# Kernel optimization log

Measured on AMD Instinct MI355X. Metric: run time of the kernel, lower is better.

## Reference

```python
import jax, jax.numpy as jnp
import numpy as np

B, N, F, D, H, L, K = 128, 128, 13, 256, 8, 8, 10
FF = 2 * D  # FFN / hidden width
HEAD = D // H


def setup_inputs() -> dict:
    key = jax.random.key(0)
    ks = iter(jax.random.split(key, 64))
    def nrm(shape, scale=0.02):
        return jax.random.normal(next(ks), shape, dtype=jnp.float32) * scale
    return {
        "input_features": jax.random.normal(next(ks), (B, N, F), dtype=jnp.float32),
        "input_points": jax.random.normal(next(ks), (B, N, 2), dtype=jnp.float32),
        "input_mask": jnp.ones((B, N, 1), dtype=jnp.float32),
        "input_time": jax.random.uniform(next(ks), (B, 1), dtype=jnp.float32),
        # get_encoding: Dense(2D, gelu) -> Dense(D, gelu)
        "enc_w1": nrm((F, FF)), "enc_b1": jnp.zeros((FF,), jnp.float32),
        "enc_w2": nrm((FF, D)), "enc_b2": jnp.zeros((D,), jnp.float32),
        # FourierProjection MLP (no bias, swish)
        "four_w1": nrm((D, FF)), "four_w2": nrm((FF, D)),
        # FiLM time projection (no bias)
        "time_w": nrm((D, FF)),
        # local KNN MLPs: round 0 input 2*F, round 1 input 2*D
        "loc1_w1": nrm((2 * F, FF)), "loc1_b1": jnp.zeros((FF,), jnp.float32),
        "loc1_w2": nrm((FF, D)), "loc1_b2": jnp.zeros((D,), jnp.float32),
        "loc2_w1": nrm((2 * D, FF)), "loc2_b1": jnp.zeros((FF,), jnp.float32),
        "loc2_w2": nrm((FF, D)), "loc2_b2": jnp.zeros((D,), jnp.float32),
        # transformer encoder layers, stacked over L
        "qkv_w": nrm((L, D, 3 * D)), "qkv_b": jnp.zeros((L, 3 * D), jnp.float32),
        "out_w": nrm((L, D, D)), "out_b": jnp.zeros((L, D), jnp.float32),
        "ln1_g": jnp.ones((L, D), jnp.float32), "ln1_b": jnp.zeros((L, D), jnp.float32),
        "ff1_w": nrm((L, D, FF)), "ff1_b": jnp.zeros((L, FF), jnp.float32),
        "ff2_w": nrm((L, FF, D)), "ff2_b": jnp.zeros((L, D), jnp.float32),
        "gamma": jnp.full((L, D), 1e-5, dtype=jnp.float32),
        "ln2_g": jnp.ones((L, D), jnp.float32), "ln2_b": jnp.zeros((L, D), jnp.float32),
    }


def _ln(x, g, b, eps=1e-5):
    m = jnp.mean(x, axis=-1, keepdims=True)
    v = jnp.var(x, axis=-1, keepdims=True)
    return (x - m) * jax.lax.rsqrt(v + eps) * g + b


def _fourier(t, w1, w2):
    # t: (B,1) -> (B,D)
    half = D // 2
    emb = np.log(10000.0) / (half - 1)
    freq = jnp.exp(-emb * jnp.arange(half, dtype=jnp.float32))
    angle = t * freq[None, :] * 1000.0  # (B, half)
    e = jnp.concatenate([jnp.sin(angle), jnp.cos(angle)], axis=-1)
    e = jax.nn.silu(e @ w1)
    return jax.nn.silu(e @ w2)


def _get_neighbors(points, feats, w1, b1, w2, b2):
    # points: (B,N,P), feats: (B,N,C) -> (B,N,D)
    r = jnp.sum(points * points, axis=-1)  # (B,N)
    d = r[:, :, None] - 2.0 * jnp.einsum('bnp,bmp->bnm', points, points) + r[:, None, :]
    _, idx = jax.lax.top_k(-d, K + 1)
    idx = idx[:, :, 1:]  # drop self, (B,N,K)
    knn = jax.vmap(lambda f, i: f[i])(feats, idx)  # (B,N,K,C)
    center = jnp.broadcast_to(feats[:, :, None, :], knn.shape)
    local = jnp.concatenate([knn - center, center], axis=-1)  # (B,N,K,2C)
    local = jax.nn.gelu(local @ w1 + b1)
    local = jax.nn.gelu(local @ w2 + b2)
    return jnp.mean(local, axis=2)


def _mha(x, mask, wqkv, bqkv, wo, bo):
    Bx, Nx, _ = x.shape
    qkv = x @ wqkv + bqkv
    q, k, v = jnp.split(qkv, 3, axis=-1)
    def heads(t):
        return t.reshape(Bx, Nx, H, HEAD).transpose(0, 2, 1, 3)
    q, k, v = heads(q), heads(k), heads(v)
    scores = jnp.einsum('bhqd,bhkd->bhqk', q, k) * (1.0 / np.sqrt(HEAD))
    keep = mask[:, None, None, :, 0] > 0  # (B,1,1,N)
    scores = jnp.where(keep, scores, -1e9)
    a = jax.nn.softmax(scores, axis=-1)
    o = jnp.einsum('bhqk,bhkd->bhqd', a, v).transpose(0, 2, 1, 3).reshape(Bx, Nx, D)
    return o @ wo + bo


def _pet(input_features, input_points, input_mask, input_time,
         enc_w1, enc_b1, enc_w2, enc_b2, four_w1, four_w2, time_w,
         loc1_w1, loc1_b1, loc1_w2, loc1_b2, loc2_w1, loc2_b1, loc2_w2, loc2_b2,
         qkv_w, qkv_b, out_w, out_b, ln1_g, ln1_b, ff1_w, ff1_b, ff2_w, ff2_b,
         gamma, ln2_g, ln2_b):
    # feature encoding (RandomDrop is identity at eval / feature_drop=0)
    enc = jax.nn.gelu(input_features @ enc_w1 + enc_b1)
    enc = jax.nn.gelu(enc @ enc_w2 + enc_b2)  # (B,N,D)
    # FiLM time conditioning
    t = _fourier(input_time, four_w1, four_w2)  # (B,D)
    t = t[:, None, :] * input_mask  # (B,N,D)
    scale, shift = jnp.split(t @ time_w, 2, axis=-1)
    enc = enc * (1.0 + scale) + shift
    # local KNN aggregation
    coord_shift = 999.0 * (1.0 - input_mask)  # (B,N,1)
    points = input_points[:, :, :2]
    lf = _get_neighbors(coord_shift + points, input_features, loc1_w1, loc1_b1, loc1_w2, loc1_b2)
    lf = _get_neighbors(coord_shift + lf, lf, loc2_w1, loc2_b1, loc2_w2, loc2_b2)
    enc = enc + lf
    skip = enc
    x = enc
    for i in range(L):
        res = x
        a = _mha(x, input_mask, qkv_w[i], qkv_b[i], out_w[i], out_b[i])
        x = _ln(res + a, ln1_g[i], ln1_b[i])
        res = x
        h = jax.nn.gelu(x @ ff1_w[i] + ff1_b[i])
        h = h @ ff2_w[i] + ff2_b[i]
        h = h * gamma[i] * input_mask  # LayerScale with mask
        x = _ln(res + h, ln2_g[i], ln2_b[i])
    return x + skip


def reference(input_features, input_points, input_mask, input_time,
              enc_w1, enc_b1, enc_w2, enc_b2, four_w1, four_w2, time_w,
              loc1_w1, loc1_b1, loc1_w2, loc1_b2, loc2_w1, loc2_b1, loc2_w2, loc2_b2,
              qkv_w, qkv_b, out_w, out_b, ln1_g, ln1_b, ff1_w, ff1_b, ff2_w, ff2_b,
              gamma, ln2_g, ln2_b):
    return _pet(input_features, input_points, input_mask, input_time,
                enc_w1, enc_b1, enc_w2, enc_b2, four_w1, four_w2, time_w,
                loc1_w1, loc1_b1, loc1_w2, loc1_b2, loc2_w1, loc2_b1, loc2_w2, loc2_b2,
                qkv_w, qkv_b, out_w, out_b, ln1_g, ln1_b, ff1_w, ff1_b, ff2_w, ff2_b,
                gamma, ln2_g, ln2_b)
```

## Files before the change

kernel.cpp:

```cpp
#include <hip/hip_runtime.h>
#include <hip/hip_bf16.h>
#include <cmath>

#define DEV_INLINE __device__ __forceinline__

constexpr int Bn = 128;
constexpr int Nn = 128;
constexpr int Fn = 13;
constexpr int Dn = 256;
constexpr int Ln = 8;
constexpr int Kn = 10;
constexpr int FFn = 512;
constexpr int Tn = Bn * Nn;
constexpr int Rn = Tn * Kn;

typedef __attribute__((ext_vector_type(4))) float f32x4;
typedef __attribute__((ext_vector_type(8))) short bf16x8;
typedef unsigned short us;

__device__ float g_x[Tn * Dn];
__device__ float g_skip[Tn * Dn];
__device__ float g_big[Tn * Dn];
__device__ float g_dm[Tn * Nn];
__device__ float g_u[Bn * FFn];
// ... 292 lines not shown
    us* Qs = (us*)(smem + 34816);
    us* Ks = (us*)(smem + 45056);
    us* Vt = (us*)(smem + 55296);
    float* msk = (float*)(smem + 64000);
    us* As = (us*)smem;
    us* Bs = (us*)(smem + 8192);
    int bh = blockIdx.x;
    int b = bh >> 3, h = bh & 7;
    int tid = threadIdx.x;
    int wave = tid >> 6, lane = tid & 63;
    int lm = lane & 15, quad = lane >> 4;
    int wm = wave << 5;
    int colu = (((lane & 3) ^ ((lane >> 2) & 3)) << 3);
    int r0 = (wave << 5) + (lane >> 2);
    const us* pa0 = xb + (size_t)(b * 128 + r0) * 256 + colu;
    const us* pa1 = xb + (size_t)(b * 128 + r0 + 16) * 256 + colu;
    int seg0 = wave, seg1 = wave + 4;
    int n0_ = seg0 * 16 + (lane >> 2);
    int n1_ = seg1 * 16 + (lane >> 2);
    int g0 = (n0_ >> 5) * 256 + h * 32 + (n0_ & 31);
    int g1 = (n1_ >> 5) * 256 + h * 32 + (n1_ & 31);
    const us* pb0 = Bt + (size_t)g0 * 256 + colu;
    const us* pb1 = Bt + (size_t)g1 * 256 + colu;
    auto lAs = (__attribute__((address_space(3))) us*)As;
    auto lBs = (__attribute__((address_space(3))) us*)Bs;
    int fcol = ((quad ^ (lm & 3)) << 3);
    f32x4 gacc[2][6] = {};
    for (int k0 = 0; k0 < 256; k0 += 32) {
        __syncthreads();
        GLOAD16(pa0 + k0, lAs + (wave << 10));
        GLOAD16(pa1 + k0, lAs + (wave << 10) + 512);
        GLOAD16(pb0 + k0, lBs + (seg0 << 9));
        if (wave < 2) GLOAD16(pb1 + k0, lBs + (seg1 << 9));
        __syncthreads();
        bf16x8 afr[2], bfr[6];
#pragma unroll
        for (int mf = 0; mf < 2; mf++)
            afr[mf] = *(const bf16x8*)&As[(wm + mf * 16 + lm) * 32 + fcol];
#pragma unroll
        for (int nf = 0; nf < 6; nf++)
            bfr[nf] = *(const bf16x8*)&Bs[(nf * 16 + lm) * 32 + fcol];
#pragma unroll
        for (int mf = 0; mf < 2; mf++)
#pragma unroll
            for (int nf = 0; nf < 6; nf++)
                gacc[mf][nf] = __builtin_amdgcn_mfma_f32_16x16x32_bf16(afr[mf], bfr[nf], gacc[mf][nf], 0, 0, 0);
    }
    float bvq[6];
#pragma unroll
    for (int nf = 0; nf < 6; nf++) {
        int n = nf * 16 + lm;
        bvq[nf] = bias[(n >> 5) * 256 + h * 32 + (n & 31)];
    }
    __syncthreads();
#pragma unroll
    for (int mf = 0; mf < 2; mf++) {
#pragma unroll
        for (int r = 0; r < 4; r++) {
            int row = wm + mf * 16 + (quad << 2) + r;
#pragma unroll
            for (int nf = 0; nf < 6; nf++) {
                us hv = f2b(gacc[mf][nf][r] + bvq[nf]);
                int n = nf * 16 + lm;
                if (nf < 2) Qs[row * 40 + n] = hv;
                else if (nf < 4) Ks[row * 40 + (n - 32)] = hv;
                else Vt[(n - 64) * 136 + row] = hv;
            }
        }
    }
    if (tid < 128) msk[tid] = mask[b * 128 + tid];
    __syncthreads();
    f32x4 acc[2][8] = {};
    {
        bf16x8 aq[2];
#pragma unroll
        for (int mf = 0; mf < 2; mf++)
            aq[mf] = *(const bf16x8*)&Qs[(wm + mf * 16 + lm) * 40 + (quad << 3)];
#pragma unroll
        for (int nf = 0; nf < 8; nf++) {
            bf16x8 bk = *(const bf16x8*)&Ks[(nf * 16 + lm) * 40 + (quad << 3)];
            acc[0][nf] = __builtin_amdgcn_mfma_f32_16x16x32_bf16(aq[0], bk, acc[0][nf], 0, 0, 0);
            acc[1][nf] = __builtin_amdgcn_mfma_f32_16x16x32_bf16(aq[1], bk, acc[1][nf], 0, 0, 0);
        }
    }
    {
        const float sc = 0.17677669529663687f;
        float mkc[8];
#pragma unroll
        for (int nf = 0; nf < 8; nf++) mkc[nf] = msk[nf * 16 + lm];
#pragma unroll
        for (int mf = 0; mf < 2; mf++) {
#pragma unroll
            for (int nf = 0; nf < 8; nf++)
#pragma unroll
                for (int r = 0; r < 4; r++) {
                    float s = acc[mf][nf][r];
                    acc[mf][nf][r] = mkc[nf] > 0.f ? s * sc : -1.0e9f;
                }
#pragma unroll
            for (int r = 0; r < 4; r++) {
                float m = acc[mf][0][r];
#pragma unroll
                for (int nf = 1; nf < 8; nf++) m = fmaxf(m, acc[mf][nf][r]);
                m = fmaxf(m, __shfl_xor(m, 1, 64));
                m = fmaxf(m, __shfl_xor(m, 2, 64));
                m = fmaxf(m, __shfl_xor(m, 4, 64));
                m = fmaxf(m, __shfl_xor(m, 8, 64));
                float s = 0.f;
#pragma unroll
                for (int nf = 0; nf < 8; nf++) {
                    float p = __expf(acc[mf][nf][r] - m);
                    acc[mf][nf][r] = p;
                    s += p;
                }
                s += __shfl_xor(s, 1, 64);
                s += __shfl_xor(s, 2, 64);
                s += __shfl_xor(s, 4, 64);
                s += __shfl_xor(s, 8, 64);
                float linv = __builtin_amdgcn_rcpf(s);
                int prow = wm + mf * 16 + (quad << 2) + r;
#pragma unroll
                for (int nf = 0; nf < 8; nf++)
                    Ps[prow * 136 + nf * 16 + lm] = f2b(acc[mf][nf][r] * linv);
            }
        }
    }
    __syncthreads();
    f32x4 oacc[2][2] = {};
    for (int kt = 0; kt < 4; kt++) {
        bf16x8 ap[2], bv[2];
#pragma unroll
        for (int mf = 0; mf < 2; mf++)
            ap[mf] = *(const bf16x8*)&Ps[(wm + mf * 16 + lm) * 136 + kt * 32 + (quad << 3)];
#pragma unroll
        for (int nf = 0; nf < 2; nf++)
            bv[nf] = *(const bf16x8*)&Vt[(nf * 16 + lm) * 136 + kt * 32 + (quad << 3)];
#pragma unroll
        for (int mf = 0; mf < 2; mf++)
#pragma unroll
            for (int nf = 0; nf < 2; nf++)
                oacc[mf][nf] = __builtin_amdgcn_mfma_f32_16x16x32_bf16(ap[mf], bv[nf], oacc[mf][nf], 0, 0, 0);
    }
#pragma unroll
    for (int mf = 0; mf < 2; mf++)
#pragma unroll
        for (int r = 0; r < 4; r++) {
            int row = wm + mf * 16 + (quad << 2) + r;
#pragma unroll
            for (int nf = 0; nf < 2; nf++)
                attb[(size_t)(b * 128 + row) * 256 + h * 32 + nf * 16 + lm] = f2b(oacc[mf][nf][r]);
        }
}

__global__ __launch_bounds__(512) void k_mglnff(const us* __restrict__ A,
                                                const us* __restrict__ Bt,
                                                const float* __restrict__ bias,
                                                const us* __restrict__ res,
                                                const float* __restrict__ lng,
                                                const float* __restrict__ lnb,
                                                const us* __restrict__ W1t,
                                                const float* __restrict__ b1,
                                                us* __restrict__ xbout,
                                                us* __restrict__ ffout) {
    __shared__ __align__(16) char smem[57856];
    us* xln = (us*)smem;
    us* As = (us*)(smem + 32768);
    us* Bs = (us*)(smem + 36864);
    us* Bs2 = (us*)(smem + 32768);
    float2* part = (float2*)(smem + 53248);
    float2* stat = (float2*)(smem + 57344);
    int tid = threadIdx.x;
    int m0 = blockIdx.x << 6;
    int wave = tid >> 6, lane = tid & 63;
    int wn = wave << 5;
    int lm = lane & 15, quad = lane >> 4;
    int colu = (((lane & 3) ^ ((lane >> 2) & 3)) << 3);
    int ar = (wave << 4) + (lane >> 2);
    int br = (wave << 5) + (lane >> 2);
    const us* pa = A + (size_t)(m0 + ar) * 256 + colu;
    const us* pb0 = Bt + (size_t)br * 256 + colu;
    const us* pb1 = Bt + (size_t)(br + 16) * 256 + colu;
    auto lAs = (__attribute__((address_space(3))) us*)As;
    auto lBs = (__attribute__((address_space(3))) us*)Bs;
    auto lBs2 = (__attribute__((address_space(3))) us*)Bs2;
    int fcol = ((quad ^ (lm & 3)) << 3);
    f32x4 acc[4][2] = {};
    for (int k0 = 0; k0 < 256; k0 += 32) {
        __syncthreads();
        if (wave < 4) GLOAD16(pa + k0, lAs + (wave << 9));
        GLOAD16(pb0 + k0, lBs + (wave << 10));
        GLOAD16(pb1 + k0, lBs + (wave << 10) + 512);
        __syncthreads();
        bf16x8 afr[4], bfr[2];
#pragma unroll
        for (int i = 0; i < 4; i++)
            afr[i] = *(const bf16x8*)&As[(i * 16 + lm) * 32 + fcol];
#pragma unroll
        for (int j = 0; j < 2; j++)
            bfr[j] = *(const bf16x8*)&Bs[(wn + j * 16 + lm) * 32 + fcol];
#pragma unroll
        for (int mf = 0; mf < 4; mf++)
#pragma unroll
            for (int nf = 0; nf < 2; nf++)
                acc[mf][nf] = __builtin_amdgcn_mfma_f32_16x16x32_bf16(afr[mf], bfr[nf], acc[mf][nf], 0, 0, 0);
    }
    float bvs[2];
#pragma unroll
    for (int nf = 0; nf < 2; nf++) bvs[nf] = bias[wn + nf * 16 + lm];
#pragma unroll
    for (int mf = 0; mf < 4; mf++) {
#pragma unroll
        for (int r = 0; r < 4; r++) {
            int rowl = mf * 16 + (quad << 2) + r;
            size_t row = (size_t)(m0 + rowl);
            float s1 = 0.f, s2 = 0.f;
#pragma unroll
            for (int nf = 0; nf < 2; nf++) {
                int col = wn + nf * 16 + lm;
                float rv = blo((unsigned)res[row * 256 + col]);
                float v = rv + acc[mf][nf][r] + bvs[nf];
                acc[mf][nf][r] = v;
                s1 += v; s2 += v * v;
            }
            s1 += __shfl_xor(s1, 1, 64); s2 += __shfl_xor(s2, 1, 64);
            s1 += __shfl_xor(s1, 2, 64); s2 += __shfl_xor(s2, 2, 64);
            s1 += __shfl_xor(s1, 4, 64); s2 += __shfl_xor(s2, 4, 64);
            s1 += __shfl_xor(s1, 8, 64); s2 += __shfl_xor(s2, 8, 64);
            if (lm == 0) { float2 p; p.x = s1; p.y = s2; part[wave * 64 + rowl] = p; }
        }
    }
    __syncthreads();
    if (tid < 64) {
        float s = 0.f, q = 0.f;
#pragma unroll
        for (int w = 0; w < 8; w++) { float2 p = part[w * 64 + tid]; s += p.x; q += p.y; }
        float mean = s * (1.f / 256.f);
        float var = q * (1.f / 256.f) - mean * mean;
        float2 st; st.x = mean; st.y = rsqrtf(var + 1e-5f);
        stat[tid] = st;
    }
    __syncthreads();
    float gvs[2], bts[2];
#pragma unroll
    for (int nf = 0; nf < 2; nf++) {
        int col = wn + nf * 16 + lm;
        gvs[nf] = lng[col];
        bts[nf] = lnb[col];
    }
#pragma unroll
    for (int mf = 0; mf < 4; mf++) {
#pragma unroll
        for (int r = 0; r < 4; r++) {
            int rowl = mf * 16 + (quad << 2) + r;
            size_t row = (size_t)(m0 + rowl);
            float2 st = stat[rowl];
#pragma unroll
            for (int nf = 0; nf < 2; nf++) {
                int col = wn + nf * 16 + lm;
                float nv = fmaf((acc[mf][nf][r] - st.x) * st.y, gvs[nf], bts[nf]);
                us hv = f2b(nv);
                xbout[row * 256 + col] = hv;
                int phys = (col >> 3) ^ (rowl & 31);
                xln[rowl * 256 + (phys << 3) + (col & 7)] = hv;
            }
        }
    }
#pragma unroll 1
    for (int nh = 0; nh < 2; nh++) {
        const us* Bt2 = W1t + (size_t)(nh * 256) * 256;
        const us* qb0 = Bt2 + (size_t)br * 256 + colu;
        const us* qb1 = Bt2 + (size_t)(br + 16) * 256 + colu;
        f32x4 acc2[4][2] = {};
        for (int k0 = 0; k0 < 256; k0 += 32) {
            __syncthreads();
            GLOAD16(qb0 + k0, lBs2 + (wave << 10));
            GLOAD16(qb1 + k0, lBs2 + (wave << 10) + 512);
            __syncthreads();
            bf16x8 afr[4], bfr[2];
#pragma unroll
            for (int i = 0; i < 4; i++) {
                int rowi = i * 16 + lm;
                int lblk = (k0 >> 3) + quad;
                int phys = lblk ^ (rowi & 31);
                afr[i] = *(const bf16x8*)&xln[rowi * 256 + (phys << 3)];
            }
#pragma unroll
            for (int j = 0; j < 2; j++)
                bfr[j] = *(const bf16x8*)&Bs2[(wn + j * 16 + lm) * 32 + fcol];
#pragma unroll
            for (int mf = 0; mf < 4; mf++)
#pragma unroll
                for (int nf = 0; nf < 2; nf++)
                    acc2[mf][nf] = __builtin_amdgcn_mfma_f32_16x16x32_bf16(afr[mf], bfr[nf], acc2[mf][nf], 0, 0, 0);
        }
        float b2v[2];
#pragma unroll
        for (int nf = 0; nf < 2; nf++) b2v[nf] = b1[nh * 256 + wn + nf * 16 + lm];
#pragma unroll
        for (int mf = 0; mf < 4; mf++) {
#pragma unroll
            for (int r = 0; r < 4; r++) {
                size_t row = (size_t)(m0 + mf * 16 + (quad << 2) + r);
#pragma unroll
                for (int nf = 0; nf < 2; nf++) {
                    float v = gelu_f(acc2[mf][nf][r] + b2v[nf]);
                    ffout[row * 512 + nh * 256 + wn + nf * 16 + lm] = f2b(v);
                }
            }
        }
    }
}

template <bool PM, bool FINAL>
__global__ __launch_bounds__(512) void k_mgln(const us* __restrict__ A,
                                              const us* __restrict__ Bt,
                                              const float* __restrict__ bias,
                                              const us* __restrict__ res,
                                              const float* __restrict__ gamma,
                                              const float* __restrict__ mask,
                                              const float* __restrict__ lng,
                                              const float* __restrict__ lnb,
                                              const float* __restrict__ skip,
                                              us* __restrict__ xbout,
                                              float* __restrict__ finout,
                                              int Kd) {
    __shared__ __align__(16) us As[64 * 32];
    __shared__ __align__(16) us Bs[256 * 32];
    __shared__ float2 part[8][64];
    __shared__ float2 stat[64];
    int tid = threadIdx.x;
    int m0 = blockIdx.x << 6;
    int wave = tid >> 6, lane = tid & 63;
    int wn = wave << 5;
    int lm = lane & 15, quad = lane >> 4;
    int colu = (((lane & 3) ^ ((lane >> 2) & 3)) << 3);
    int ar = (wave << 4) + (lane >> 2);
    int br = (wave << 5) + (lane >> 2);
    const us* pa = A + (size_t)(m0 + ar) * Kd + colu;
    const us* pb0 = Bt + (size_t)br * Kd + colu;
    const us* pb1 = Bt + (size_t)(br + 16) * Kd + colu;
    auto lAs = (__attribute__((address_space(3))) us*)As;
    auto lBs = (__attribute__((address_space(3))) us*)Bs;
    int fcol = ((quad ^ (lm & 3)) << 3);
    f32x4 acc[4][2] = {};
    for (int k0 = 0; k0 < Kd; k0 += 32) {
        __syncthreads();
        if (wave < 4) GLOAD16(pa + k0, lAs + (wave << 9));
        GLOAD16(pb0 + k0, lBs + (wave << 10));
        GLOAD16(pb1 + k0, lBs + (wave << 10) + 512);
        __syncthreads();
        bf16x8 afr[4], bfr[2];
#pragma unroll
        for (int i = 0; i < 4; i++)
            afr[i] = *(const bf16x8*)&As[(i * 16 + lm) * 32 + fcol];
#pragma unroll
        for (int j = 0; j < 2; j++)
            bfr[j] = *(const bf16x8*)&Bs[(wn + j * 16 + lm) * 32 + fcol];
#pragma unroll
        for (int mf = 0; mf < 4; mf++)
#pragma unroll
            for (int nf = 0; nf < 2; nf++)
                acc[mf][nf] = __builtin_amdgcn_mfma_f32_16x16x32_bf16(afr[mf], bfr[nf], acc[mf][nf], 0, 0, 0);
    }
    float bvs[2], gms[2];
#pragma unroll
    for (int nf = 0; nf < 2; nf++) {
        int col = wn + nf * 16 + lm;
        bvs[nf] = bias[col];
        if (PM) gms[nf] = gamma[col];
    }
#pragma unroll
    for (int mf = 0; mf < 4; mf++) {
#pragma unroll
        for (int r = 0; r < 4; r++) {
            int rowl = mf * 16 + (quad << 2) + r;
            size_t row = (size_t)(m0 + rowl);
            float mrow = PM ? mask[row] : 0.f;
            float s1 = 0.f, s2 = 0.f;
#pragma unroll
            for (int nf = 0; nf < 2; nf++) {
                int col = wn + nf * 16 + lm;
                float rv = blo((unsigned)res[row * 256 + col]);
                float v = acc[mf][nf][r] + bvs[nf];
                v = PM ? fmaf(v * gms[nf], mrow, rv) : rv + v;
                acc[mf][nf][r] = v;
                s1 += v; s2 += v * v;
            }
            s1 += __shfl_xor(s1, 1, 64); s2 += __shfl_xor(s2, 1, 64);
            s1 += __shfl_xor(s1, 2, 64); s2 += __shfl_xor(s2, 2, 64);
            s1 += __shfl_xor(s1, 4, 64); s2 += __shfl_xor(s2, 4, 64);
            s1 += __shfl_xor(s1, 8, 64); s2 += __shfl_xor(s2, 8, 64);
            if (lm == 0) { float2 p; p.x = s1; p.y = s2; part[wave][rowl] = p; }
        }
    }
    __syncthreads();
    if (tid < 64) {
        float s = 0.f, q = 0.f;
#pragma unroll
        for (int w = 0; w < 8; w++) { float2 p = part[w][tid]; s += p.x; q += p.y; }
        float mean = s * (1.f / 256.f);
        float var = q * (1.f / 256.f) - mean * mean;
        float2 st; st.x = mean; st.y = rsqrtf(var + 1e-5f);
        stat[tid] = st;
    }
    __syncthreads();
    float gvs[2], bts[2];
#pragma unroll
    for (int nf = 0; nf < 2; nf++) {
        int col = wn + nf * 16 + lm;
        gvs[nf] = lng[col];
        bts[nf] = lnb[col];
    }
#pragma unroll
    for (int mf = 0; mf < 4; mf++) {
#pragma unroll
        for (int r = 0; r < 4; r++) {
            int rowl = mf * 16 + (quad << 2) + r;
            size_t row = (size_t)(m0 + rowl);
            float2 st = stat[rowl];
#pragma unroll
            for (int nf = 0; nf < 2; nf++) {
                int col = wn + nf * 16 + lm;
                float nv = fmaf((acc[mf][nf][r] - st.x) * st.y, gvs[nf], bts[nf]);
                if (FINAL) finout[row * 256 + col] = nv + skip[row * 256 + col];
                else xbout[row * 256 + col] = f2b(nv);
            }
        }
    }
}

__global__ __launch_bounds__(512) void k_knng(const us* __restrict__ pq,
                                              const int* __restrict__ idx,
                                              const us* __restrict__ Bt,
                                              const float* __restrict__ bias,
                                              us* __restrict__ h2b) {
    __shared__ __align__(16) us As[128 * 64];
    __shared__ __align__(16) us Bs[256 * 64];
    int tid = threadIdx.x;
    int m0 = blockIdx.x << 7;
    int wave = tid >> 6, lane = tid & 63;
    int wm = (wave & 1) << 6, wn = (wave >> 1) << 6;
    int lm = lane & 15, quad = lane >> 4;
    int arow = tid >> 2, acolu = (tid & 3) << 4;
    int asw = arow & 7;
    int ablk0 = ((tid & 3) << 1) ^ asw, ablk1 = (((tid & 3) << 1) + 1) ^ asw;
    int r = m0 + arow;
    int tok = r / 10;
    int nb = idx[r];
    int prow = (tok & ~127) + nb;
    const us* Pp = pq + (size_t)prow * 1024 + acolu;
    const us* Qp = pq + (size_t)tok * 1024 + 512 + acolu;
    int brow = (wave << 5) + (lane >> 3);
    int bcol = (((lane & 7) ^ (lane >> 3)) << 3);
    const us* pb = Bt + (size_t)brow * 512 + bcol;
    auto lBs = (__attribute__((address_space(3))) us*)Bs;
    int lbase = wave << 11;
    int fsw = lm & 7;
    f32x4 acc[4][4] = {};
    for (int k0 = 0; k0 < 512; k0 += 64) {
        uint4 pv0 = *(const uint4*)(Pp + k0);
        uint4 pv1 = *(const uint4*)(Pp + k0 + 8);
        uint4 qv0 = *(const uint4*)(Qp + k0);
        uint4 qv1 = *(const uint4*)(Qp + k0 + 8);
        uint4 h0, h1;
        h0.x = pk2(gelu_f(blo(pv0.x) + blo(qv0.x)), gelu_f(bhi(pv0.x) + bhi(qv0.x)));
        h0.y = pk2(gelu_f(blo(pv0.y) + blo(qv0.y)), gelu_f(bhi(pv0.y) + bhi(qv0.y)));
        h0.z = pk2(gelu_f(blo(pv0.z) + blo(qv0.z)), gelu_f(bhi(pv0.z) + bhi(qv0.z)));
        h0.w = pk2(gelu_f(blo(pv0.w) + blo(qv0.w)), gelu_f(bhi(pv0.w) + bhi(qv0.w)));
        h1.x = pk2(gelu_f(blo(pv1.x) + blo(qv1.x)), gelu_f(bhi(pv1.x) + bhi(qv1.x)));
        h1.y = pk2(gelu_f(blo(pv1.y) + blo(qv1.y)), gelu_f(bhi(pv1.y) + bhi(qv1.y)));
        h1.z = pk2(gelu_f(blo(pv1.z) + blo(qv1.z)), gelu_f(bhi(pv1.z) + bhi(qv1.z)));
        h1.w = pk2(gelu_f(blo(pv1.w) + blo(qv1.w)), gelu_f(bhi(pv1.w) + bhi(qv1.w)));
        __syncthreads();
        GLOAD16(pb + k0, lBs + lbase);
        GLOAD16(pb + k0 + 8 * 512, lBs + lbase + 512);
        GLOAD16(pb + k0 + 16 * 512, lBs + lbase + 1024);
        GLOAD16(pb + k0 + 24 * 512, lBs + lbase + 1536);
        *(uint4*)&As[arow * 64 + (ablk0 << 3)] = h0;
        *(uint4*)&As[arow * 64 + (ablk1 << 3)] = h1;
        __syncthreads();
#pragma unroll
        for (int sub = 0; sub < 2; sub++) {
            int lblk = (sub << 2) + quad;
            int fcol = ((lblk ^ fsw) << 3);
            bf16x8 afr[4], bfr[4];
#pragma unroll
            for (int i = 0; i < 4; i++) {
                afr[i] = *(const bf16x8*)&As[(wm + i * 16 + lm) * 64 + fcol];
                bfr[i] = *(const bf16x8*)&Bs[(wn + i * 16 + lm) * 64 + fcol];
            }
#pragma unroll
            for (int mf = 0; mf < 4; mf++)
#pragma unroll
                for (int nf = 0; nf < 4; nf++)
                    acc[mf][nf] = __builtin_amdgcn_mfma_f32_16x16x32_bf16(afr[mf], bfr[nf], acc[mf][nf], 0, 0, 0);
        }
    }
    float bvs[4];
#pragma unroll
    for (int nf = 0; nf < 4; nf++) bvs[nf] = bias[wn + nf * 16 + lm];
#pragma unroll
    for (int mf = 0; mf < 4; mf++) {
#pragma unroll
        for (int rr = 0; rr < 4; rr++) {
            size_t row = (size_t)(m0 + wm + mf * 16 + (quad << 2) + rr);
#pragma unroll
            for (int nf = 0; nf < 4; nf++) {
                float v = gelu_f(acc[mf][nf][rr] + bvs[nf]);
                h2b[row * 256 + wn + nf * 16 + lm] = f2b(v);
            }
        }
    }
}

__global__ __launch_bounds__(64) void k_mean1s(const us* __restrict__ h2b,
                                               const float* __restrict__ mask,
                                               us* __restrict__ lfb,
                                               float* __restrict__ big,
                                               float* __restrict__ r) {
    int t = blockIdx.x, lane = threadIdx.x;
    int c = lane << 2;
    const us* p = h2b + (size_t)t * Kn * 256 + c;
    float s0 = 0.f, s1 = 0.f, s2 = 0.f, s3 = 0.f;
#pragma unroll
    for (int k = 0; k < Kn; k++) {
        uint2 v = *(const uint2*)(p + k * 256);
        s0 += blo(v.x); s1 += bhi(v.x);
        s2 += blo(v.y); s3 += bhi(v.y);
    }
    s0 *= 0.1f; s1 *= 0.1f; s2 *= 0.1f; s3 *= 0.1f;
    uint2 ob; ob.x = pk2(s0, s1); ob.y = pk2(s2, s3);
    *(uint2*)&lfb[(size_t)t * 256 + c] = ob;
    float sh = 999.f * (1.f - mask[t]);
    float4 w; w.x = s0 + sh; w.y = s1 + sh; w.z = s2 + sh; w.w = s3 + sh;
    *(float4*)&big[(size_t)t * 256 + c] = w;
    float sq = w.x * w.x + w.y * w.y + w.z * w.z + w.w * w.w;
#pragma unroll
    for (int off = 32; off; off >>= 1) sq += __shfl_xor(sq, off, 64);
    if (lane == 0) r[t] = sq;
}

__global__ __launch_bounds__(256) void k_dist(const float* __restrict__ fe,
                                              const float* __restrict__ r,
                                              float* __restrict__ Dm) {
    int b = blockIdx.z;
    int m0 = blockIdx.x * 64, n0 = blockIdx.y * 64;
    const float* A = fe + (size_t)b * Nn * Dn;
    __shared__ float As[16][68];
    __shared__ float Bs[16][68];
    int tid = threadIdx.x;
    int tx = tid & 15, ty = tid >> 4;
    int ar = tid >> 2, ac = (tid & 3) << 2;
    float acc[4][4] = {};
    for (int k0 = 0; k0 < Dn; k0 += 16) {
        float4 av = *(const float4*)&A[(size_t)(n0 + ar) * Dn + k0 + ac];
        float4 bv = *(const float4*)&A[(size_t)(m0 + ar) * Dn + k0 + ac];
        __syncthreads();
        As[ac + 0][ar] = av.x; As[ac + 1][ar] = av.y; As[ac + 2][ar] = av.z; As[ac + 3][ar] = av.w;
        Bs[ac + 0][ar] = bv.x; Bs[ac + 1][ar] = bv.y; Bs[ac + 2][ar] = bv.z; Bs[ac + 3][ar] = bv.w;
        __syncthreads();
#pragma unroll
        for (int kk = 0; kk < 16; kk++) {
            float4 a = *(const float4*)&As[kk][ty << 2];
            float4 b2 = *(const float4*)&Bs[kk][tx << 2];
            acc[0][0] += a.x * b2.x; acc[0][1] += a.x * b2.y; acc[0][2] += a.x * b2.z; acc[0][3] += a.x * b2.w;
            acc[1][0] += a.y * b2.x; acc[1][1] += a.y * b2.y; acc[1][2] += a.y * b2.z; acc[1][3] += a.y * b2.w;
            acc[2][0] += a.z * b2.x; acc[2][1] += a.z * b2.y; acc[2][2] += a.z * b2.z; acc[2][3] += a.z * b2.w;
            acc[3][0] += a.w * b2.x; acc[3][1] += a.w * b2.y; acc[3][2] += a.w * b2.z; acc[3][3] += a.w * b2.w;
        }
    }
    float4 rm = *(const float4*)&r[b * Nn + m0 + (tx << 2)];
#pragma unroll
    for (int i = 0; i < 4; i++) {
        int n = n0 + (ty << 2) + i;
        float rn = r[b * Nn + n];
        float4 v;
        v.x = rn - 2.f * acc[i][0] + rm.x;
        v.y = rn - 2.f * acc[i][1] + rm.y;
        v.z = rn - 2.f * acc[i][2] + rm.z;
        v.w = rn - 2.f * acc[i][3] + rm.w;
        *(float4*)&Dm[(size_t)b * Nn * Nn + (size_t)n * Nn + m0 + (tx << 2)] = v;
    }
}

__global__ __launch_bounds__(128) void k_topkg(const float* __restrict__ Dm, int* __restrict__ idx) {
    int b = blockIdx.x, n = threadIdx.x;
    const float* row = Dm + (size_t)b * Nn * Nn + (size_t)n * Nn;
    float bd[Kn + 1]; int bi[Kn + 1];
#pragma unroll
    for (int j = 0; j <= Kn; j++) { bd[j] = 3.4e38f; bi[j] = -1; }
    for (int m = 0; m < Nn; m++) {
        float d = row[m];
        if (d < bd[Kn]) {
            int j = Kn;
            while (j > 0 && d < bd[j - 1]) { bd[j] = bd[j - 1]; bi[j] = bi[j - 1]; j--; }
            bd[j] = d; bi[j] = m;
        }
    }
    for (int j = 1; j <= Kn; j++) idx[(size_t)(b * Nn + n) * Kn + j - 1] = bi[j];
}

__global__ __launch_bounds__(256) void k_meanc(const us* __restrict__ h2b,
                                               const float* __restrict__ u,
                                               const float* __restrict__ mask,
                                               const float* __restrict__ x,
                                               float* __restrict__ skip,
                                               us* __restrict__ xb) {
    int t = blockIdx.x, c = threadIdx.x;
    const us* p = h2b + (size_t)t * Kn * 256 + c;
    float s = 0.f;
#pragma unroll
    for (int k = 0; k < Kn; k++) s += blo((unsigned)p[k * 256]);
    s *= 0.1f;
    int b = t >> 7;
    float m = mask[t];
    float xv = x[(size_t)t * Dn + c];
    float sc = u[(size_t)b * 512 + c];
    float sh = u[(size_t)b * 512 + 256 + c];
    float v = xv * (1.f + m * sc) + m * sh + s;
    skip[(size_t)t * Dn + c] = v;
    xb[(size_t)t * Dn + c] = f2b(v);
}

extern "C" void kernel_launch(void* const* d_in, const int* in_sizes, int n_in,
                              void* d_out, int out_size, void* d_ws, size_t ws_size,
                              hipStream_t stream) {
    (void)in_sizes; (void)n_in; (void)out_size; (void)d_ws; (void)ws_size;
    const float* f_feat = (const float*)d_in[0];
    const float* f_pts  = (const float*)d_in[1];
    const float* f_mask = (const float*)d_in[2];
    const float* f_time = (const float*)d_in[3];
    const float* enc_w1 = (const float*)d_in[4];
    const float* enc_b1 = (const float*)d_in[5];
    const float* enc_w2 = (const float*)d_in[6];
    const float* enc_b2 = (const float*)d_in[7];
    const float* four_w1 = (const float*)d_in[8];
    const float* four_w2 = (const float*)d_in[9];
    const float* time_w = (const float*)d_in[10];
    const float* l1w1 = (const float*)d_in[11];
    const float* l1b1 = (const float*)d_in[12];
    const float* l1w2 = (const float*)d_in[13];
    const float* l1b2 = (const float*)d_in[14];
    const float* l2w1 = (const float*)d_in[15];
    const float* l2b1 = (const float*)d_in[16];
    const float* l2w2 = (const float*)d_in[17];
    const float* l2b2 = (const float*)d_in[18];
    const float* qkv_w = (const float*)d_in[19];
    const float* qkv_b = (const float*)d_in[20];
    const float* out_w = (const float*)d_in[21];
    const float* out_b = (const float*)d_in[22];
    const float* ln1g = (const float*)d_in[23];
    const float* ln1b = (const float*)d_in[24];
    const float* ff1w = (const float*)d_in[25];
    const float* ff1b = (const float*)d_in[26];
    const float* ff2w = (const float*)d_in[27];
    const float* ff2b = (const float*)d_in[28];
    const float* gam  = (const float*)d_in[29];
    const float* ln2g = (const float*)d_in[30];
    const float* ln2b = (const float*)d_in[31];
    float* out = (float*)d_out;

    float *x, *skip, *big, *dm, *u, *r, *pqbias;
    int* idx;
    us *bigb, *xb, *attb, *lf1b, *pq, *h2b, *feat16, *wt;
    hipGetSymbolAddress((void**)&x,    HIP_SYMBOL(g_x));
    hipGetSymbolAddress((void**)&skip, HIP_SYMBOL(g_skip));
    hipGetSymbolAddress((void**)&big,  HIP_SYMBOL(g_big));
    hipGetSymbolAddress((void**)&dm,   HIP_SYMBOL(g_dm));
    hipGetSymbolAddress((void**)&u,    HIP_SYMBOL(g_u));
    hipGetSymbolAddress((void**)&r,    HIP_SYMBOL(g_r));
    hipGetSymbolAddress((void**)&pqbias, HIP_SYMBOL(g_pqbias));
    hipGetSymbolAddress((void**)&idx,  HIP_SYMBOL(g_idx));
    hipGetSymbolAddress((void**)&bigb, HIP_SYMBOL(g_bigb));
    hipGetSymbolAddress((void**)&xb,   HIP_SYMBOL(g_xb));
    hipGetSymbolAddress((void**)&attb, HIP_SYMBOL(g_attb));
    hipGetSymbolAddress((void**)&lf1b, HIP_SYMBOL(g_lf1b));
    hipGetSymbolAddress((void**)&pq,   HIP_SYMBOL(g_pq));
    hipGetSymbolAddress((void**)&h2b,  HIP_SYMBOL(g_h2b));
    hipGetSymbolAddress((void**)&feat16, HIP_SYMBOL(g_feat16));
    hipGetSymbolAddress((void**)&wt,   HIP_SYMBOL(g_wt));

    k_uprep<<<UPN, 256, 0, stream>>>(
        enc_w1, enc_w2, l1w2, l2w2, qkv_w, out_w, ff1w, ff2w,
        l1w1, l1b1, l2w1, l2b1, f_feat, f_time, four_w1, four_w2, time_w,
        f_pts, f_mask, wt, pqbias, feat16, u, idx);

    k_mg2<1, true><<<dim3(4, 128), 256, 0, stream>>>(feat16, wt + OFF_ENC1, enc_b1, bigb, 32, 512);
    k_mg2<1, false><<<dim3(2, 128), 256, 0, stream>>>(bigb, wt + OFF_ENC2, enc_b2, x, 512, 256);
    k_mg2<0, true><<<dim3(8, 128), 256, 0, stream>>>(feat16, wt + OFF_PQ1, pqbias, pq, 32, 1024);
    k_knng<<<Rn / 128, 512, 0, stream>>>(pq, idx, wt + OFF_W2A, l1b2, h2b);
    k_mean1s<<<Tn, 64, 0, stream>>>(h2b, f_mask, lf1b, big, r);
    k_dist<<<dim3(2, 2, Bn), 256, 0, stream>>>(big, r, dm);
    k_topkg<<<Bn, Nn, 0, stream>>>(dm, idx);
    k_mg2<0, true><<<dim3(8, 128), 256, 0, stream>>>(lf1b, wt + OFF_PQ2, pqbias + 1024, pq, 256, 1024);
    k_knng<<<Rn / 128, 512, 0, stream>>>(pq, idx, wt + OFF_W2B, l2b2, h2b);
    k_meanc<<<Tn, 256, 0, stream>>>(h2b, u, f_mask, x, skip, xb);
    for (int l = 0; l < Ln; l++) {
        k_qattn<<<Bn * 8, 256, 0, stream>>>(
            xb, wt + OFF_QKV + (size_t)l * 768 * 256, qkv_b + l * 768, f_mask, attb);
        k_mglnff<<<256, 512, 0, stream>>>(
            attb, wt + OFF_OUT + (size_t)l * 256 * 256, out_b + l * 256,
            xb, ln1g + l * Dn, ln1b + l * Dn,
            wt + OFF_FF1 + (size_t)l * 512 * 256, ff1b + l * 512, xb, bigb);
        if (l < Ln - 1)
            k_mgln<true, false><<<256, 512, 0, stream>>>(
                bigb, wt + OFF_FF2 + (size_t)l * 256 * 512, ff2b + l * 256,
                xb, gam + l * Dn, f_mask, ln2g + l * Dn, ln2b + l * Dn, nullptr, xb, nullptr, 512);
        else
            k_mgln<true, true><<<256, 512, 0, stream>>>(
                bigb, wt + OFF_FF2 + (size_t)l * 256 * 512, ff2b + l * 256,
                xb, gam + l * Dn, f_mask, ln2g + l * Dn, ln2b + l * Dn, skip, nullptr, out, 512);
    }
}
```

Measured before the change: 1.301 ms.

## Fuse out-proj, LN1, FF1, FF2 and LN2 into one per-layer kernel

Merges the two per-layer kernels into a single k_ffn kernel. It runs the attention output projection plus LN1, FF1 with GELU, and FF2 with LayerScale, mask and LN2 per 32-row tile. The GELU hidden activations stay in swizzled LDS instead of making a round trip through global memory, and one launch per layer is removed. To fit shared memory the M tile drops from 64 to 32 rows and the grid doubles to 512 blocks. Each block therefore reloads every weight matrix for half as many rows, which doubles weight traffic from L2.

```diff
diff --git a/kernel.cpp b/kernel.cpp
--- a/kernel.cpp
+++ b/kernel.cpp
@@ -468,278 +468,260 @@
         }
 }
 
-__global__ __launch_bounds__(512) void k_mglnff(const us* __restrict__ A,
-                                                const us* __restrict__ Bt,
-                                                const float* __restrict__ bias,
-                                                const us* __restrict__ res,
-                                                const float* __restrict__ lng,
-                                                const float* __restrict__ lnb,
-                                                const us* __restrict__ W1t,
-                                                const float* __restrict__ b1,
-                                                us* __restrict__ xbout,
-                                                us* __restrict__ ffout) {
-    __shared__ __align__(16) char smem[57856];
+template <bool FINAL>
+__global__ __launch_bounds__(512) void k_ffn(const us* __restrict__ A,
+                                             const us* __restrict__ Wout,
+                                             const float* __restrict__ bout,
+                                             const us* __restrict__ res,
+                                             const float* __restrict__ ln1gv,
+                                             const float* __restrict__ ln1bv,
+                                             const us* __restrict__ W1t,
+                                             const float* __restrict__ b1,
+                                             const us* __restrict__ W2t,
+                                             const float* __restrict__ b2,
+                                             const float* __restrict__ gamma,
+                                             const float* __restrict__ mask,
+                                             const float* __restrict__ ln2gv,
+                                             const float* __restrict__ ln2bv,
+                                             const float* __restrict__ skip,
+                                             us* __restrict__ xbout,
+                                             float* __restrict__ finout) {
+    __shared__ __align__(16) char smem[65536];
     us* xln = (us*)smem;
-    us* As = (us*)(smem + 32768);
-    us* Bs = (us*)(smem + 36864);
-    us* Bs2 = (us*)(smem + 32768);
-    float2* part = (float2*)(smem + 53248);
-    float2* stat = (float2*)(smem + 57344);
+    us* hS  = (us*)(smem + 16384);
+    us* Bs  = (us*)(smem + 49152);
+    us* As  = (us*)(smem + 16384);
+    float2* part = (float2*)(smem + 18432);
+    float2* stat = (float2*)(smem + 20480);
     int tid = threadIdx.x;
-    int m0 = blockIdx.x << 6;
+    int m0 = blockIdx.x << 5;
     int wave = tid >> 6, lane = tid & 63;
     int wn = wave << 5;
     int lm = lane & 15, quad = lane >> 4;
     int colu = (((lane & 3) ^ ((lane >> 2) & 3)) << 3);
     int ar = (wave << 4) + (lane >> 2);
     int br = (wave << 5) + (lane >> 2);
-    const us* pa = A + (size_t)(m0 + ar) * 256 + colu;
-    const us* pb0 = Bt + (size_t)br * 256 + colu;
-    const us* pb1 = Bt + (size_t)(br + 16) * 256 + colu;
     auto lAs = (__attribute__((address_space(3))) us*)As;
     auto lBs = (__attribute__((address_space(3))) us*)Bs;
-    auto lBs2 = (__attribute__((address_space(3))) us*)Bs2;
     int fcol = ((quad ^ (lm & 3)) << 3);
-    f32x4 acc[4][2] = {};
-    for (int k0 = 0; k0 < 256; k0 += 32) {
-        __syncthreads();
-        if (wave < 4) GLOAD16(pa + k0, lAs + (wave << 9));
-        GLOAD16(pb0 + k0, lBs + (wave << 10));
-        GLOAD16(pb1 + k0, lBs + (wave << 10) + 512);
-        __syncthreads();
-        bf16x8 afr[4], bfr[2];
-#pragma unroll
-        for (int i = 0; i < 4; i++)
-            afr[i] = *(const bf16x8*)&As[(i * 16 + lm) * 32 + fcol];
-#pragma unroll
-        for (int j = 0; j < 2; j++)
-            bfr[j] = *(const bf16x8*)&Bs[(wn + j * 16 + lm) * 32 + fcol];
-#pragma unroll
-        for (int mf = 0; mf < 4; mf++)
-#pragma unroll
-            for (int nf = 0; nf < 2; nf++)
-                acc[mf][nf] = __builtin_amdgcn_mfma_f32_16x16x32_bf16(afr[mf], bfr[nf], acc[mf][nf], 0, 0, 0);
-    }
-    float bvs[2];
-#pragma unroll
-    for (int nf = 0; nf < 2; nf++) bvs[nf] = bias[wn + nf * 16 + lm];
-#pragma unroll
-    for (int mf = 0; mf < 4; mf++) {
-#pragma unroll
-        for (int r = 0; r < 4; r++) {
-            int rowl = mf * 16 + (quad << 2) + r;
-            size_t row = (size_t)(m0 + rowl);
-            float s1 = 0.f, s2 = 0.f;
-#pragma unroll
-            for (int nf = 0; nf < 2; nf++) {
-                int col = wn + nf * 16 + lm;
-                float rv = blo((unsigned)res[row * 256 + col]);
-                float v = rv + acc[mf][nf][r] + bvs[nf];
-                acc[mf][nf][r] = v;
-                s1 += v; s2 += v * v;
-            }
-            s1 += __shfl_xor(s1, 1, 64); s2 += __shfl_xor(s2, 1, 64);
-            s1 += __shfl_xor(s1, 2, 64); s2 += __shfl_xor(s2, 2, 64);
-            s1 += __shfl_xor(s1, 4, 64); s2 += __shfl_xor(s2, 4, 64);
-            s1 += __shfl_xor(s1, 8, 64); s2 += __shfl_xor(s2, 8, 64);
-            if (lm == 0) { float2 p; p.x = s1; p.y = s2; part[wave * 64 + rowl] = p; }
-        }
-    }
-    __syncthreads();
-    if (tid < 64) {
-        float s = 0.f, q = 0.f;
-#pragma unroll
-        for (int w = 0; w < 8; w++) { float2 p = part[w * 64 + tid]; s += p.x; q += p.y; }
-        float mean = s * (1.f / 256.f);
-        float var = q * (1.f / 256.f) - mean * mean;
-        float2 st; st.x = mean; st.y = rsqrtf(var + 1e-5f);
-        stat[tid] = st;
-    }
-    __syncthreads();
-    float gvs[2], bts[2];
-#pragma unroll
-    for (int nf = 0; nf < 2; nf++) {
-        int col = wn + nf * 16 + lm;
-        gvs[nf] = lng[col];
-        bts[nf] = lnb[col];
-    }
-#pragma unroll
-    for (int mf = 0; mf < 4; mf++) {
-#pragma unroll
-        for (int r = 0; r < 4; r++) {
-            int rowl = mf * 16 + (quad << 2) + r;
-            size_t row = (size_t)(m0 + rowl);
-            float2 st = stat[rowl];
-#pragma unroll
-            for (int nf = 0; nf < 2; nf++) {
-                int col = wn + nf * 16 + lm;
-                float nv = fmaf((acc[mf][nf][r] - st.x) * st.y, gvs[nf], bts[nf]);
-                us hv = f2b(nv);
-                xbout[row * 256 + col] = hv;
-                int phys = (col >> 3) ^ (rowl & 31);
-                xln[rowl * 256 + (phys << 3) + (col & 7)] = hv;
-            }
-        }
+    {
+        const us* pa = A + (size_t)(m0 + ar) * 256 + colu;
+        const us* pb0 = Wout + (size_t)br * 256 + colu;
+        const us* pb1 = Wout + (size_t)(br + 16) * 256 + colu;
+        f32x4 acc[2][2] = {};
+        for (int k0 = 0; k0 < 256; k0 += 32) {
+            __syncthreads();
+            if (wave < 2) GLOAD16(pa + k0, lAs + (wave << 9));
+            GLOAD16(pb0 + k0, lBs + (wave << 10));
+            GLOAD16(pb1 + k0, lBs + (wave << 10) + 512);
+            __syncthreads();
+            bf16x8 afr[2], bfr[2];
+#pragma unroll
+            for (int i = 0; i < 2; i++)
+                afr[i] = *(const bf16x8*)&As[(i * 16 + lm) * 32 + fcol];
+#pragma unroll
+            for (int j = 0; j < 2; j++)
+                bfr[j] = *(const bf16x8*)&Bs[(wn + j * 16 + lm) * 32 + fcol];
+#pragma unroll
+            for (int mf = 0; mf < 2; mf++)
+#pragma unroll
+                for (int nf = 0; nf < 2; nf++)
+                    acc[mf][nf] = __builtin_amdgcn_mfma_f32_16x16x32_bf16(afr[mf], bfr[nf], acc[mf][nf], 0, 0, 0);
+        }
+        float bvs[2];
+#pragma unroll
+        for (int nf = 0; nf < 2; nf++) bvs[nf] = bout[wn + nf * 16 + lm];
+#pragma unroll
+        for (int mf = 0; mf < 2; mf++) {
+#pragma unroll
+            for (int r = 0; r < 4; r++) {
+                int rowl = mf * 16 + (quad << 2) + r;
+                size_t row = (size_t)(m0 + rowl);
+                float s1 = 0.f, s2 = 0.f;
+#pragma unroll
+                for (int nf = 0; nf < 2; nf++) {
+                    int col = wn + nf * 16 + lm;
+                    float rv = blo((unsigned)res[row * 256 + col]);
+                    float v = rv + acc[mf][nf][r] + bvs[nf];
+                    acc[mf][nf][r] = v;
+                    s1 += v; s2 += v * v;
+                }
+                s1 += __shfl_xor(s1, 1, 64); s2 += __shfl_xor(s2, 1, 64);
+                s1 += __shfl_xor(s1, 2, 64); s2 += __shfl_xor(s2, 2, 64);
+                s1 += __shfl_xor(s1, 4, 64); s2 += __shfl_xor(s2, 4, 64);
+                s1 += __shfl_xor(s1, 8, 64); s2 += __shfl_xor(s2, 8, 64);
+                if (lm == 0) { float2 p; p.x = s1; p.y = s2; part[wave * 32 + rowl] = p; }
+            }
+        }
+        __syncthreads();
+        if (tid < 32) {
+            float s = 0.f, q = 0.f;
+#pragma unroll
+            for (int w = 0; w < 8; w++) { float2 p = part[w * 32 + tid]; s += p.x; q += p.y; }
+            float mean = s * (1.f / 256.f);
+            float var = q * (1.f / 256.f) - mean * mean;
+            float2 st; st.x = mean; st.y = rsqrtf(var + 1e-5f);
+            stat[tid] = st;
+        }
+        __syncthreads();
+        float gvs[2], bts[2];
+#pragma unroll
+        for (int nf = 0; nf < 2; nf++) {
+            int col = wn + nf * 16 + lm;
+            gvs[nf] = ln1gv[col];
+            bts[nf] = ln1bv[col];
+        }
+#pragma unroll
+        for (int mf = 0; mf < 2; mf++) {
+#pragma unroll
+            for (int r = 0; r < 4; r++) {
+                int rowl = mf * 16 + (quad << 2) + r;
+                float2 st = stat[rowl];
+#pragma unroll
+                for (int nf = 0; nf < 2; nf++) {
+                    int col = wn + nf * 16 + lm;
+                    float nv = fmaf((acc[mf][nf][r] - st.x) * st.y, gvs[nf], bts[nf]);
+                    int phys = (col >> 3) ^ rowl;
+                    xln[rowl * 256 + (phys << 3) + (col & 7)] = f2b(nv);
+                }
+            }
+        }
+        __syncthreads();
     }
 #pragma unroll 1
     for (int nh = 0; nh < 2; nh++) {
         const us* Bt2 = W1t + (size_t)(nh * 256) * 256;
         const us* qb0 = Bt2 + (size_t)br * 256 + colu;
         const us* qb1 = Bt2 + (size_t)(br + 16) * 256 + colu;
-        f32x4 acc2[4][2] = {};
+        f32x4 acc2[2][2] = {};
         for (int k0 = 0; k0 < 256; k0 += 32) {
             __syncthreads();
-            GLOAD16(qb0 + k0, lBs2 + (wave << 10));
-            GLOAD16(qb1 + k0, lBs2 + (wave << 10) + 512);
+            GLOAD16(qb0 + k0, lBs + (wave << 10));
+            GLOAD16(qb1 + k0, lBs + (wave << 10) + 512);
             __syncthreads();
-            bf16x8 afr[4], bfr[2];
-#pragma unroll
-            for (int i = 0; i < 4; i++) {
+            bf16x8 afr[2], bfr[2];
+#pragma unroll
+            for (int i = 0; i < 2; i++) {
                 int rowi = i * 16 + lm;
-                int lblk = (k0 >> 3) + quad;
-                int phys = lblk ^ (rowi & 31);
+                int phys = ((k0 >> 3) + quad) ^ rowi;
                 afr[i] = *(const bf16x8*)&xln[rowi * 256 + (phys << 3)];
             }
 #pragma unroll
             for (int j = 0; j < 2; j++)
-                bfr[j] = *(const bf16x8*)&Bs2[(wn + j * 16 + lm) * 32 + fcol];
-#pragma unroll
-            for (int mf = 0; mf < 4; mf++)
+                bfr[j] = *(const bf16x8*)&Bs[(wn + j * 16 + lm) * 32 + fcol];
+#pragma unroll
+            for (int mf = 0; mf < 2; mf++)
 #pragma unroll
                 for (int nf = 0; nf < 2; nf++)
                     acc2[mf][nf] = __builtin_amdgcn_mfma_f32_16x16x32_bf16(afr[mf], bfr[nf], acc2[mf][nf], 0, 0, 0);
         }
-        float b2v[2];
-#pragma unroll
-        for (int nf = 0; nf < 2; nf++) b2v[nf] = b1[nh * 256 + wn + nf * 16 + lm];
-#pragma unroll
-        for (int mf = 0; mf < 4; mf++) {
+        float b1v[2];
+#pragma unroll
+        for (int nf = 0; nf < 2; nf++) b1v[nf] = b1[nh * 256 + wn + nf * 16 + lm];
+#pragma unroll
+        for (int mf = 0; mf < 2; mf++) {
 #pragma unroll
             for (int r = 0; r < 4; r++) {
-                size_t row = (size_t)(m0 + mf * 16 + (quad << 2) + r);
+                int rowl = mf * 16 + (quad << 2) + r;
 #pragma unroll
                 for (int nf = 0; nf < 2; nf++) {
-                    float v = gelu_f(acc2[mf][nf][r] + b2v[nf]);
-                    ffout[row * 512 + nh * 256 + wn + nf * 16 + lm] = f2b(v);
+                    int gcol = nh * 256 + wn + nf * 16 + lm;
+                    float v = gelu_f(acc2[mf][nf][r] + b1v[nf]);
+                    int phys = (gcol >> 3) ^ rowl;
+                    hS[rowl * 512 + (phys << 3) + (gcol & 7)] = f2b(v);
                 }
             }
         }
     }
-}
-
-template <bool PM, bool FINAL>
-__global__ __launch_bounds__(512) void k_mgln(const us* __restrict__ A,
-                                              const us* __restrict__ Bt,
-                                              const float* __restrict__ bias,
-                                              const us* __restrict__ res,
-                                              const float* __restrict__ gamma,
-                                              const float* __restrict__ mask,
-                                              const float* __restrict__ lng,
-                                              const float* __restrict__ lnb,
-                                              const float* __restrict__ skip,
-                                              us* __restrict__ xbout,
-                                              float* __restrict__ finout,
-                                              int Kd) {
-    __shared__ __align__(16) us As[64 * 32];
-    __shared__ __align__(16) us Bs[256 * 32];
-    __shared__ float2 part[8][64];
-    __shared__ float2 stat[64];
-    int tid = threadIdx.x;
-    int m0 = blockIdx.x << 6;
-    int wave = tid >> 6, lane = tid & 63;
-    int wn = wave << 5;
-    int lm = lane & 15, quad = lane >> 4;
-    int colu = (((lane & 3) ^ ((lane >> 2) & 3)) << 3);
-    int ar = (wave << 4) + (lane >> 2);
-    int br = (wave << 5) + (lane >> 2);
-    const us* pa = A + (size_t)(m0 + ar) * Kd + colu;
-    const us* pb0 = Bt + (size_t)br * Kd + colu;
-    const us* pb1 = Bt + (size_t)(br + 16) * Kd + colu;
-    auto lAs = (__attribute__((address_space(3))) us*)As;
-    auto lBs = (__attribute__((address_space(3))) us*)Bs;
-    int fcol = ((quad ^ (lm & 3)) << 3);
-    f32x4 acc[4][2] = {};
-    for (int k0 = 0; k0 < Kd; k0 += 32) {
-        __syncthreads();
-        if (wave < 4) GLOAD16(pa + k0, lAs + (wave << 9));
-        GLOAD16(pb0 + k0, lBs + (wave << 10));
-        GLOAD16(pb1 + k0, lBs + (wave << 10) + 512);
-        __syncthreads();
-        bf16x8 afr[4], bfr[2];
-#pragma unroll
-        for (int i = 0; i < 4; i++)
-            afr[i] = *(const bf16x8*)&As[(i * 16 + lm) * 32 + fcol];
-#pragma unroll
-        for (int j = 0; j < 2; j++)
-            bfr[j] = *(const bf16x8*)&Bs[(wn + j * 16 + lm) * 32 + fcol];
-#pragma unroll
-        for (int mf = 0; mf < 4; mf++)
-#pragma unroll
-            for (int nf = 0; nf < 2; nf++)
-                acc[mf][nf] = __builtin_amdgcn_mfma_f32_16x16x32_bf16(afr[mf], bfr[nf], acc[mf][nf], 0, 0, 0);
-    }
-    float bvs[2], gms[2];
-#pragma unroll
-    for (int nf = 0; nf < 2; nf++) {
-        int col = wn + nf * 16 + lm;
-        bvs[nf] = bias[col];
-        if (PM) gms[nf] = gamma[col];
-    }
-#pragma unroll
-    for (int mf = 0; mf < 4; mf++) {
-#pragma unroll
-        for (int r = 0; r < 4; r++) {
-            int rowl = mf * 16 + (quad << 2) + r;
-            size_t row = (size_t)(m0 + rowl);
-            float mrow = PM ? mask[row] : 0.f;
-            float s1 = 0.f, s2 = 0.f;
-#pragma unroll
-            for (int nf = 0; nf < 2; nf++) {
-                int col = wn + nf * 16 + lm;
-                float rv = blo((unsigned)res[row * 256 + col]);
-                float v = acc[mf][nf][r] + bvs[nf];
-                v = PM ? fmaf(v * gms[nf], mrow, rv) : rv + v;
-                acc[mf][nf][r] = v;
-                s1 += v; s2 += v * v;
-            }
-            s1 += __shfl_xor(s1, 1, 64); s2 += __shfl_xor(s2, 1, 64);
-            s1 += __shfl_xor(s1, 2, 64); s2 += __shfl_xor(s2, 2, 64);
-            s1 += __shfl_xor(s1, 4, 64); s2 += __shfl_xor(s2, 4, 64);
-            s1 += __shfl_xor(s1, 8, 64); s2 += __shfl_xor(s2, 8, 64);
-            if (lm == 0) { float2 p; p.x = s1; p.y = s2; part[wave][rowl] = p; }
-        }
-    }
-    __syncthreads();
-    if (tid < 64) {
-        float s = 0.f, q = 0.f;
-#pragma unroll
-        for (int w = 0; w < 8; w++) { float2 p = part[w][tid]; s += p.x; q += p.y; }
-        float mean = s * (1.f / 256.f);
-        float var = q * (1.f / 256.f) - mean * mean;
-        float2 st; st.x = mean; st.y = rsqrtf(var + 1e-5f);
-        stat[tid] = st;
-    }
-    __syncthreads();
-    float gvs[2], bts[2];
-#pragma unroll
-    for (int nf = 0; nf < 2; nf++) {
-        int col = wn + nf * 16 + lm;
-        gvs[nf] = lng[col];
-        bts[nf] = lnb[col];
-    }
-#pragma unroll
-    for (int mf = 0; mf < 4; mf++) {
-#pragma unroll
-        for (int r = 0; r < 4; r++) {
-            int rowl = mf * 16 + (quad << 2) + r;
-            size_t row = (size_t)(m0 + rowl);
-            float2 st = stat[rowl];
-#pragma unroll
-            for (int nf = 0; nf < 2; nf++) {
-                int col = wn + nf * 16 + lm;
-                float nv = fmaf((acc[mf][nf][r] - st.x) * st.y, gvs[nf], bts[nf]);
-                if (FINAL) finout[row * 256 + col] = nv + skip[row * 256 + col];
-                else xbout[row * 256 + col] = f2b(nv);
+    {
+        const us* pc0 = W2t + (size_t)br * 512 + colu;
+        const us* pc1 = W2t + (size_t)(br + 16) * 512 + colu;
+        f32x4 acc3[2][2] = {};
+        for (int k0 = 0; k0 < 512; k0 += 32) {
+            __syncthreads();
+            GLOAD16(pc0 + k0, lBs + (wave << 10));
+            GLOAD16(pc1 + k0, lBs + (wave << 10) + 512);
+            __syncthreads();
+            bf16x8 afr[2], bfr[2];
+#pragma unroll
+            for (int i = 0; i < 2; i++) {
+                int rowi = i * 16 + lm;
+                int phys = ((k0 >> 3) + quad) ^ rowi;
+                afr[i] = *(const bf16x8*)&hS[rowi * 512 + (phys << 3)];
+            }
+#pragma unroll
+            for (int j = 0; j < 2; j++)
+                bfr[j] = *(const bf16x8*)&Bs[(wn + j * 16 + lm) * 32 + fcol];
+#pragma unroll
+            for (int mf = 0; mf < 2; mf++)
+#pragma unroll
+                for (int nf = 0; nf < 2; nf++)
+                    acc3[mf][nf] = __builtin_amdgcn_mfma_f32_16x16x32_bf16(afr[mf], bfr[nf], acc3[mf][nf], 0, 0, 0);
+        }
+        __syncthreads();
+        float b2v[2], gmv[2];
+#pragma unroll
+        for (int nf = 0; nf < 2; nf++) {
+            int col = wn + nf * 16 + lm;
+            b2v[nf] = b2[col];
+            gmv[nf] = gamma[col];
+        }
+#pragma unroll
+        for (int mf = 0; mf < 2; mf++) {
+#pragma unroll
+            for (int r = 0; r < 4; r++) {
+                int rowl = mf * 16 + (quad << 2) + r;
+                size_t row = (size_t)(m0 + rowl);
+                float mrow = mask[row];
+                float s1 = 0.f, s2 = 0.f;
+#pragma unroll
+                for (int nf = 0; nf < 2; nf++) {
+                    int col = wn + nf * 16 + lm;
+                    int phys = (col >> 3) ^ rowl;
+                    float xv = blo((unsigned)xln[rowl * 256 + (phys << 3) + (col & 7)]);
+                    float v = fmaf((acc3[mf][nf][r] + b2v[nf]) * gmv[nf], mrow, xv);
+                    acc3[mf][nf][r] = v;
+                    s1 += v; s2 += v * v;
+                }
+                s1 += __shfl_xor(s1, 1, 64); s2 += __shfl_xor(s2, 1, 64);
+                s1 += __shfl_xor(s1, 2, 64); s2 += __shfl_xor(s2, 2, 64);
+                s1 += __shfl_xor(s1, 4, 64); s2 += __shfl_xor(s2, 4, 64);
+                s1 += __shfl_xor(s1, 8, 64); s2 += __shfl_xor(s2, 8, 64);
+                if (lm == 0) { float2 p; p.x = s1; p.y = s2; part[wave * 32 + rowl] = p; }
+            }
+        }
+        __syncthreads();
+        if (tid < 32) {
+            float s = 0.f, q = 0.f;
+#pragma unroll
+            for (int w = 0; w < 8; w++) { float2 p = part[w * 32 + tid]; s += p.x; q += p.y; }
+            float mean = s * (1.f / 256.f);
+            float var = q * (1.f / 256.f) - mean * mean;
+            float2 st; st.x = mean; st.y = rsqrtf(var + 1e-5f);
+            stat[tid] = st;
+        }
+        __syncthreads();
+        float gvs[2], bts[2];
+#pragma unroll
+        for (int nf = 0; nf < 2; nf++) {
+            int col = wn + nf * 16 + lm;
+            gvs[nf] = ln2gv[col];
+            bts[nf] = ln2bv[col];
+        }
+#pragma unroll
+        for (int mf = 0; mf < 2; mf++) {
+#pragma unroll
+            for (int r = 0; r < 4; r++) {
+                int rowl = mf * 16 + (quad << 2) + r;
+                size_t row = (size_t)(m0 + rowl);
+                float2 st = stat[rowl];
+#pragma unroll
+                for (int nf = 0; nf < 2; nf++) {
+                    int col = wn + nf * 16 + lm;
+                    float nv = fmaf((acc3[mf][nf][r] - st.x) * st.y, gvs[nf], bts[nf]);
+                    if (FINAL) finout[row * 256 + col] = nv + skip[row * 256 + col];
+                    else xbout[row * 256 + col] = f2b(nv);
+                }
             }
         }
     }
@@ -1014,17 +996,21 @@
     for (int l = 0; l < Ln; l++) {
         k_qattn<<<Bn * 8, 256, 0, stream>>>(
             xb, wt + OFF_QKV + (size_t)l * 768 * 256, qkv_b + l * 768, f_mask, attb);
-        k_mglnff<<<256, 512, 0, stream>>>(
-            attb, wt + OFF_OUT + (size_t)l * 256 * 256, out_b + l * 256,
-            xb, ln1g + l * Dn, ln1b + l * Dn,
-            wt + OFF_FF1 + (size_t)l * 512 * 256, ff1b + l * 512, xb, bigb);
         if (l < Ln - 1)
-            k_mgln<true, false><<<256, 512, 0, stream>>>(
-                bigb, wt + OFF_FF2 + (size_t)l * 256 * 512, ff2b + l * 256,
-                xb, gam + l * Dn, f_mask, ln2g + l * Dn, ln2b + l * Dn, nullptr, xb, nullptr, 512);
+            k_ffn<false><<<512, 512, 0, stream>>>(
+                attb, wt + OFF_OUT + (size_t)l * 256 * 256, out_b + l * 256,
+                xb, ln1g + l * Dn, ln1b + l * Dn,
+                wt + OFF_FF1 + (size_t)l * 512 * 256, ff1b + l * 512,
+                wt + OFF_FF2 + (size_t)l * 256 * 512, ff2b + l * 256,
+                gam + l * Dn, f_mask, ln2g + l * Dn, ln2b + l * Dn,
+                nullptr, xb, nullptr);
         else
-            k_mgln<true, true><<<256, 512, 0, stream>>>(
-                bigb, wt + OFF_FF2 + (size_t)l * 256 * 512, ff2b + l * 256,
-                xb, gam + l * Dn, f_mask, ln2g + l * Dn, ln2b + l * Dn, skip, nullptr, out, 512);
-    }
-}
+            k_ffn<true><<<512, 512, 0, stream>>>(
+                attb, wt + OFF_OUT + (size_t)l * 256 * 256, out_b + l * 256,
+                xb, ln1g + l * Dn, ln1b + l * Dn,
+                wt + OFF_FF1 + (size_t)l * 512 * 256, ff1b + l * 512,
+                wt + OFF_FF2 + (size_t)l * 256 * 512, ff2b + l * 256,
+                gam + l * Dn, f_mask, ln2g + l * Dn, ln2b + l * Dn,
+                skip, nullptr, out);
+    }
+}
```

Result: slower. 1.351 ms (+3.9%).
